# Optimization experiments

Hardware: AMD Instinct MI355X
Metric: run time of the kernel (lower is better)

## Reference

```python
import jax, jax.numpy as jnp
import numpy as np

C, INTER, RED4 = 256, 128, 64  # in_channels, inter_ch=max(C//2,32), C//4

def setup_inputs() -> dict:
    key = jax.random.key(0)
    ks = jax.random.split(key, 12)
    B, H, W = 8, 64, 64
    s = 0.02
    return {
        "x": jax.random.normal(ks[0], (B, C, H, W), dtype=jnp.float32),
        "theta_w": jax.random.normal(ks[1], (INTER, C), dtype=jnp.float32) * s,
        "phi_w": jax.random.normal(ks[2], (INTER, C), dtype=jnp.float32) * s,
        "g_w": jax.random.normal(ks[3], (INTER, C), dtype=jnp.float32) * s,
        "out_w": jax.random.normal(ks[4], (C, INTER), dtype=jnp.float32) * s,
        "bn_gamma": jnp.ones((C,), dtype=jnp.float32),
        "bn_beta": jnp.zeros((C,), dtype=jnp.float32),
        "fc1_w": jax.random.normal(ks[5], (RED4, C), dtype=jnp.float32) * s,
        "fc1_b": jnp.zeros((RED4,), dtype=jnp.float32),
        "fc2_w": jax.random.normal(ks[6], (C, RED4), dtype=jnp.float32) * s,
        "fc2_b": jnp.zeros((C,), dtype=jnp.float32),
    }

def reference(x, theta_w, phi_w, g_w, out_w, bn_gamma, bn_beta, fc1_w, fc1_b, fc2_w, fc2_b):
    B, Cc, H, W = x.shape
    N = H * W
    xf = x.reshape(B, Cc, N)                              # [B,C,N]
    # 1x1 convs == per-pixel matmuls
    theta = jnp.einsum('ic,bcn->bni', theta_w, xf)        # [B,N,I]
    phi = jnp.einsum('ic,bcn->bin', phi_w, xf)            # [B,I,N]
    g = jnp.einsum('ic,bcn->bni', g_w, xf)                # [B,N,I]
    scale = 1.0 / jnp.sqrt(jnp.asarray(theta.shape[-1], theta.dtype))
    attn = jax.nn.softmax(jnp.einsum('bni,bim->bnm', theta, phi) * scale, axis=-1)  # [B,N,N]
    out = jnp.einsum('bnm,bmi->bni', attn, g)             # [B,N,I]
    out = jnp.einsum('ci,bni->bcn', out_w, out).reshape(B, Cc, H, W)
    # BatchNorm2d (training mode: batch stats, biased variance, eps=1e-5)
    mean = out.mean(axis=(0, 2, 3))
    var = out.var(axis=(0, 2, 3))
    out = (out - mean[:, None, None]) * jax.lax.rsqrt(var[:, None, None] + 1e-5)
    out = out * bn_gamma[:, None, None] + bn_beta[:, None, None]
    # SE channel attention on the input x
    pooled = x.mean(axis=(2, 3))                          # [B,C]
    h = jax.nn.relu(pooled @ fc1_w.T + fc1_b)
    ch_w = jax.nn.sigmoid(h @ fc2_w.T + fc2_b)[:, :, None, None]
    return x + out * ch_w
```

## Files before the change

### kernel.cpp

```cpp
#include <hip/hip_runtime.h>

#define B_DIM 8
#define C_DIM 256
#define I_DIM 128
#define N_DIM 4096
#define R_DIM 64

typedef unsigned short u16;
typedef unsigned int u32;
typedef __attribute__((ext_vector_type(8))) __bf16 bf16x8;
typedef __attribute__((ext_vector_type(4))) float f32x4;
typedef __attribute__((ext_vector_type(16))) float f32x16;

union BF8 { u32 u[4]; bf16x8 v; };

__device__ __forceinline__ u16 f2bf(float f) {
    union { float f; u32 u; } v; v.f = f;
    u32 r = v.u + 0x7FFFu + ((v.u >> 16) & 1u);
    return (u16)(r >> 16);
}
__device__ __forceinline__ float bf2f(u16 h) {
    union { u32 u; float f; } v; v.u = (u32)h << 16; return v.f;
}
__device__ __forceinline__ u32 pk2(float a, float b) {
    return (u32)f2bf(a) | ((u32)f2bf(b) << 16);
}
__device__ __forceinline__ u32 pk2t(float a, float b) {
    union { float f; u32 u; } ua, ub; ua.f = a; ub.f = b;
    return __builtin_amdgcn_perm(ub.u, ua.u, 0x07060302u);
}
__device__ __forceinline__ void async16(const u16* g, u16* l) {
    __builtin_amdgcn_global_load_lds((const __attribute__((address_space(1))) void*)g,
                                     (__attribute__((address_space(3))) void*)l, 16, 0, 0);
}

#define TH_SCALE 0.1275204890136f

static constexpr size_t OFF_BNSUM = 0;
static constexpr size_t OFF_BNSQ  = 1024;
static constexpr size_t OFF_POOL  = 2048;
static constexpr size_t OFF_CHW   = 10240;
static constexpr size_t OFF_W3    = 18432;
static constexpr size_t OFF_OWB   = 215040;
static constexpr size_t OFF_AO0   = 280576;
static constexpr size_t OFF_AO1   = OFF_AO0 + 8388608;
static constexpr size_t OFF_THETA = OFF_AO1 + 8388608;
static constexpr size_t OFF_PHIT  = OFF_THETA + 8388608;
static constexpr size_t OFF_GT    = OFF_PHIT + 8388608;
static constexpr size_t OFF_L0    = OFF_GT + 8388608;
static constexpr size_t OFF_L1    = OFF_L0 + 131072;
static constexpr size_t OFF_OUT2  = OFF_L1 + 131072;

__global__ void prep_kernel(const float* __restrict__ tw, const float* __restrict__ pw,
                            const float* __restrict__ gw, const float* __restrict__ ow,
                            u16* __restrict__ w3, u16* __restrict__ owb,
                            float* __restrict__ bnzero, float* __restrict__ pooled) {
    int idx = blockIdx.x * 256 + threadIdx.x;
    if (idx < 512) bnzero[idx] = 0.f;
    if (idx < 2048) pooled[idx] = 0.f;
    if (idx < 3 * 32768) {
        const float* src = idx < 32768 ? tw : (idx < 65536 ? pw : gw);
        w3[idx] = f2bf(src[idx & 32767]);
    }
    if (idx < 32768) owb[idx] = f2bf(ow[idx]);
}

__global__ void se_kernel(const float* __restrict__ pooled,
                          const float* __restrict__ fc1w, const float* __restrict__ fc1b,
                          const float* __restrict__ fc2w, const float* __restrict__ fc2b,
                          float* __restrict__ chw) {
    int b = blockIdx.x, t = threadIdx.x;
    __shared__ float sp[C_DIM], sh[R_DIM];
    sp[t] = pooled[b * C_DIM + t] * (1.f / N_DIM);
    __syncthreads();
    if (t < R_DIM) {
        float a = fc1b[t];
        for (int c = 0; c < C_DIM; ++c) a += sp[c] * fc1w[t * C_DIM + c];
        sh[t] = a > 0.f ? a : 0.f;
    }
    __syncthreads();
    float a = fc2b[t];
    for (int j = 0; j < R_DIM; ++j) a += sh[j] * fc2w[t * R_DIM + j];
    chw[b * C_DIM + t] = 1.f / (1.f + __builtin_amdgcn_exp2f(-a * 1.44269504089f));
}

__global__ __launch_bounds__(256) void qkv_kernel(const float* __restrict__ x,
                                                  const u16* __restrict__ w3,
                                                  u16* __restrict__ theta,
                                                  u16* __restrict__ phiT,
                                                  u16* __restrict__ gT,
                                                  float* __restrict__ pooled) {
    const int bid = blockIdx.x;
    const int b = bid & 7, nt = bid >> 3;
    const int n0 = nt * 64;
    const int t = threadIdx.x, lane = t & 63, w = t >> 6;
    const int cl = lane & 31, h = lane >> 5;

    __shared__ u16 As[64 * 256];
    __shared__ u16 Ep[128 * 72];

    {
        const float* xb = x + ((size_t)b * C_DIM) * N_DIM + n0;
        for (int it = 0; it < 16; ++it) {
            int id = it * 256 + t;
            int c = id >> 4, l16 = id & 15;
            float4 v = *(const float4*)(xb + (size_t)c * N_DIM + l16 * 4);
            int g = c >> 3, co = c & 7;
            float vv[4] = {v.x, v.y, v.z, v.w};
            #pragma unroll
            for (int k = 0; k < 4; ++k) {
                int n = l16 * 4 + k;
                As[n * 256 + ((g ^ (n & 7)) << 3) + co] = f2bf(vv[k]);
            }
            float s = (v.x + v.y) + (v.z + v.w);
            s += __shfl_xor(s, 1); s += __shfl_xor(s, 2);
            s += __shfl_xor(s, 4); s += __shfl_xor(s, 8);
            if ((t & 15) == 0) atomicAdd(&pooled[b * C_DIM + c], s);
        }
    }
    __syncthreads();

    const int mt = w & 1;
    const int ip = w >> 1;
    bf16x8 afr[16];
    #pragma unroll
    for (int ks = 0; ks < 16; ++ks) {
        int r = mt * 32 + cl;
        int g = 2 * ks + h;
        afr[ks] = *(const bf16x8*)&As[r * 256 + ((g ^ (r & 7)) << 3)];
    }

    for (int z = 0; z < 3; ++z) {
        const u16* wz = w3 + z * (I_DIM * C_DIM);
        f32x16 acc[2] = {};
        #pragma unroll
        for (int ks = 0; ks < 16; ++ks) {
            #pragma unroll
            for (int f = 0; f < 2; ++f) {
                int irow = (2 * ip + f) * 32 + cl;
                bf16x8 bfr = *(const bf16x8*)(wz + (size_t)irow * C_DIM + ks * 16 + h * 8);
                acc[f] = __builtin_amdgcn_mfma_f32_32x32x16_bf16(afr[ks], bfr, acc[f], 0, 0, 0);
            }
        }
        if (z < 2) {
            float sc = (z == 0) ? TH_SCALE : 1.0f;
            #pragma unroll
            for (int f = 0; f < 2; ++f) {
                int i = (2 * ip + f) * 32 + cl;
                #pragma unroll
                for (int r2 = 0; r2 < 4; ++r2)
                    #pragma unroll
                    for (int e = 0; e < 4; ++e) {
                        int n = mt * 32 + 8 * r2 + 4 * h + e;
                        Ep[n * 136 + i] = f2bf(acc[f][4 * r2 + e] * sc);
                    }
            }
            __syncthreads();
            u16* dst = (z == 0) ? theta : phiT;
            #pragma unroll
            for (int it = 0; it < 4; ++it) {
                int id = it * 256 + t;
                int n = id >> 4, l16 = id & 15;
                f32x4 vv = *(const f32x4*)&Ep[n * 136 + l16 * 8];
                *(f32x4*)(dst + ((size_t)(b * N_DIM) + n0 + n) * I_DIM + l16 * 8) = vv;
            }
            __syncthreads();
        } else {
            #pragma unroll
            for (int f = 0; f < 2; ++f) {
                int i = (2 * ip + f) * 32 + cl;
                #pragma unroll
                for (int r2 = 0; r2 < 4; ++r2) {
                    u32 lo = pk2(acc[f][4 * r2 + 0], acc[f][4 * r2 + 1]);
                    u32 hi = pk2(acc[f][4 * r2 + 2], acc[f][4 * r2 + 3]);
                    int nb = mt * 32 + 8 * r2 + 4 * h;
                    *(u32*)&Ep[i * 72 + nb] = lo;
                    *(u32*)&Ep[i * 72 + nb + 2] = hi;
                }
            }
            __syncthreads();
            #pragma unroll
            for (int it = 0; it < 4; ++it) {
                int id = it * 256 + t;
                int i = id >> 3, l8 = id & 7;
                f32x4 vv = *(const f32x4*)&Ep[i * 72 + l8 * 8];
                *(f32x4*)(gT + ((size_t)(b * I_DIM) + i) * N_DIM + n0 + l8 * 8) = vv;
            }
        }
    }
}

__global__ __launch_bounds__(256) void attn_kernel(const u16* __restrict__ theta,
                                                   const u16* __restrict__ phiT,
                                                   const u16* __restrict__ gT,
                                                   u16* __restrict__ ao0, u16* __restrict__ ao1,
                                                   float* __restrict__ l0, float* __restrict__ l1) {
    const int bid = blockIdx.x;
    const int b = bid & 7, mh = (bid >> 3) & 1, qt = bid >> 4;
    const int t = threadIdx.x, lane = t & 63, w = t >> 6;
    const int cl = lane & 31, h = lane >> 5;
    const int qw = qt * 128 + w * 32;

    __shared__ u16 SM[32768];
    __shared__ float lex[4][32];

    bf16x8 qf[8];
    {
        const u16* qp = theta + ((size_t)(b * N_DIM) + qw + cl) * I_DIM + h * 8;
        #pragma unroll
        for (int ks = 0; ks < 8; ++ks) qf[ks] = *(const bf16x8*)(qp + ks * 16);
    }

    const u16* kbase = phiT + (size_t)b * N_DIM * I_DIM + (size_t)(mh * 2048) * I_DIM;
    const u16* vbase = gT + (size_t)b * I_DIM * N_DIM + mh * 2048;
    const u16* kptr[4]; const u16* vptr[4];
    #pragma unroll
    for (int it = 0; it < 4; ++it) {
        int gi = (w * 4 + it) * 64 + lane;
        int kr = gi >> 4, kg = gi & 15;
        kptr[it] = kbase + (size_t)kr * I_DIM + ((kg ^ (kr & 7)) << 3);
        int vr = gi >> 3, vg = gi & 7;
        vptr[it] = vbase + (size_t)vr * N_DIM + ((vg ^ (vr & 7)) << 3);
    }

    auto issue = [&](int p) {
        u16* Kd = SM + p * 16384;
        u16* Vd = SM + p * 16384 + 8192;
        #pragma unroll
        for (int it = 0; it < 4; ++it) { async16(kptr[it], Kd + (w * 4 + it) * 512); kptr[it] += 64 * I_DIM; }
        #pragma unroll
        for (int it = 0; it < 4; ++it) { async16(vptr[it], Vd + (w * 4 + it) * 512); vptr[it] += 64; }
    };

    float lsum = 0.f;
    f32x16 O[4] = {};

    issue(0);

    for (int mc = 0; mc < 32; ++mc) {
        const int p = mc & 1;
        __asm__ volatile("s_barrier" ::: "memory");
        if (mc < 31) {
            issue(1 - p);
            __asm__ volatile("s_waitcnt vmcnt(8)" ::: "memory");
        } else {
            __asm__ volatile("s_waitcnt vmcnt(0)" ::: "memory");
        }
        __asm__ volatile("s_barrier" ::: "memory");

        const u16* Ks = SM + p * 16384;
        const u16* Vs = SM + p * 16384 + 8192;

        u32 pk[8][2];
        #pragma unroll
        for (int mt2 = 0; mt2 < 2; ++mt2) {
            f32x16 S = {};
            #pragma unroll
            for (int ks = 0; ks < 8; ++ks) {
                int r = mt2 * 32 + cl;
                bf16x8 kf = *(const bf16x8*)&Ks[r * 128 + (((2 * ks + h) ^ (r & 7)) << 3)];
                S = __builtin_amdgcn_mfma_f32_32x32x16_bf16(kf, qf[ks], S, 0, 0, 0);
            }
            #pragma unroll
            for (int r2 = 0; r2 < 4; ++r2) {
                float p0 = __builtin_amdgcn_exp2f(S[4 * r2 + 0]);
                float p1 = __builtin_amdgcn_exp2f(S[4 * r2 + 1]);
                float p2 = __builtin_amdgcn_exp2f(S[4 * r2 + 2]);
                float p3 = __builtin_amdgcn_exp2f(S[4 * r2 + 3]);
                lsum += (p0 + p1) + (p2 + p3);
                pk[mt2 * 4 + r2][0] = pk2t(p0, p1);
                pk[mt2 * 4 + r2][1] = pk2t(p2, p3);
            }
        }

        #pragma unroll
        for (int ks = 0; ks < 4; ++ks) {
            u32 a0 = pk[2 * ks][0], a1 = pk[2 * ks][1];
            u32 b0 = pk[2 * ks + 1][0], b1 = pk[2 * ks + 1][1];
            bool hb = (h != 0);
            u32 own0 = hb ? b0 : a0, own1 = hb ? b1 : a1;
            u32 xf0 = hb ? a0 : b0, xf1 = hb ? a1 : b1;
            u32 rc0 = (u32)__shfl_xor((int)xf0, 32);
            u32 rc1 = (u32)__shfl_xor((int)xf1, 32);
            BF8 A;
            A.u[0] = hb ? rc0 : own0;
            A.u[1] = hb ? rc1 : own1;
            A.u[2] = hb ? own0 : rc0;
            A.u[3] = hb ? own1 : rc1;
            #pragma unroll
            for (int f = 0; f < 4; ++f) {
                int ir = f * 32 + cl;
                bf16x8 vf = *(const bf16x8*)&Vs[ir * 64 + (((2 * ks + h) ^ (ir & 7)) << 3)];
                O[f] = __builtin_amdgcn_mfma_f32_32x32x16_bf16(A.v, vf, O[f], 0, 0, 0);
            }
        }
    }

    lsum += __shfl_xor(lsum, 32);
    if (h == 0) lex[w][cl] = lsum;
    __asm__ volatile("s_waitcnt lgkmcnt(0)" ::: "memory");

    float linv[16];
    {
        float* lw = lex[w];
        #pragma unroll
        for (int r2 = 0; r2 < 4; ++r2) {
            f32x4 lv = *(const f32x4*)&lw[8 * r2 + 4 * h];
            #pragma unroll
            for (int e = 0; e < 4; ++e) linv[4 * r2 + e] = 1.f / lv[e];
        }
    }

    u16* aop = (mh == 0) ? ao0 : ao1;
    float* lp = (mh == 0) ? l0 : l1;
    if (h == 0) lp[(size_t)b * N_DIM + qw + cl] = lsum;

    u16* ep = SM + w * 4096;
    #pragma unroll
    for (int f = 0; f < 4; ++f)
        #pragma unroll
        for (int r2 = 0; r2 < 4; ++r2)
            #pragma unroll
            for (int e = 0; e < 4; ++e) {
                int q = 8 * r2 + 4 * h + e;
                ep[q * 128 + f * 32 + cl] = f2bf(O[f][4 * r2 + e] * linv[4 * r2 + e]);
            }
    __asm__ volatile("s_waitcnt lgkmcnt(0)" ::: "memory");
    #pragma unroll
    for (int it = 0; it < 8; ++it) {
        int id = it * 64 + lane;
        int q = id >> 4, l16 = id & 15;
        f32x4 vv = *(const f32x4*)&ep[q * 128 + l16 * 8];
        *(f32x4*)(aop + ((size_t)(b * N_DIM) + qw + q) * I_DIM + l16 * 8) = vv;
    }
}

__global__ __launch_bounds__(256) void oproj_kernel(const u16* __restrict__ ao0,
                                                    const u16* __restrict__ ao1,
                                                    const float* __restrict__ l0,
                                                    const float* __restrict__ l1,
                                                    const u16* __restrict__ owb,
                                                    u16* __restrict__ out2,
                                                    float* __restrict__ bnsum,
                                                    float* __restrict__ bnsumsq) {
    const int bid = blockIdx.x;
    const int b = bid & 7, nt = bid >> 3;
    const int n0 = nt * 64;
    const int t = threadIdx.x, lane = t & 63, w = t >> 6;
    const int cl = lane & 31, h = lane >> 5;

    __shared__ u16 Ep[256 * 72];
    __shared__ float lsum[C_DIM], lsq[C_DIM];
    lsum[t] = 0.f; lsq[t] = 0.f;
    __syncthreads();

    const int mt = w & 1;
    const int nn = n0 + mt * 32 + cl;
    float w0, w1;
    {
        float la = l0[(size_t)b * N_DIM + nn], lb = l1[(size_t)b * N_DIM + nn];
        float inv = 1.f / (la + lb);
        w0 = la * inv; w1 = lb * inv;
    }
    bf16x8 afr[8];
    {
        const u16* p0 = ao0 + ((size_t)(b * N_DIM) + nn) * I_DIM + h * 8;
        const u16* p1 = ao1 + ((size_t)(b * N_DIM) + nn) * I_DIM + h * 8;
        #pragma unroll
        for (int ks = 0; ks < 8; ++ks) {
            bf16x8 x0 = *(const bf16x8*)(p0 + ks * 16);
            bf16x8 x1 = *(const bf16x8*)(p1 + ks * 16);
            const u16* u0 = (const u16*)&x0;
            const u16* u1 = (const u16*)&x1;
            float c0 = w0 * bf2f(u0[0]) + w1 * bf2f(u1[0]);
            float c1 = w0 * bf2f(u0[1]) + w1 * bf2f(u1[1]);
            float c2 = w0 * bf2f(u0[2]) + w1 * bf2f(u1[2]);
            float c3 = w0 * bf2f(u0[3]) + w1 * bf2f(u1[3]);
            float c4 = w0 * bf2f(u0[4]) + w1 * bf2f(u1[4]);
            float c5 = w0 * bf2f(u0[5]) + w1 * bf2f(u1[5]);
            float c6 = w0 * bf2f(u0[6]) + w1 * bf2f(u1[6]);
            float c7 = w0 * bf2f(u0[7]) + w1 * bf2f(u1[7]);
            BF8 r;
            r.u[0] = pk2(c0, c1); r.u[1] = pk2(c2, c3);
            r.u[2] = pk2(c4, c5); r.u[3] = pk2(c6, c7);
            afr[ks] = r.v;
        }
    }

    f32x16 D[4] = {};
    #pragma unroll
    for (int ks = 0; ks < 8; ++ks) {
        #pragma unroll
        for (int j = 0; j < 4; ++j) {
            int cr = ((w >> 1) * 4 + j) * 32 + cl;
            bf16x8 bfr = *(const bf16x8*)(owb + (size_t)cr * I_DIM + ks * 16 + h * 8);
            D[j] = __builtin_amdgcn_mfma_f32_32x32x16_bf16(afr[ks], bfr, D[j], 0, 0, 0);
        }
    }

    #pragma unroll
    for (int j = 0; j < 4; ++j) {
        int c = ((w >> 1) * 4 + j) * 32 + cl;
        float s1 = 0.f, s2 = 0.f;
        #pragma unroll
        for (int r2 = 0; r2 < 4; ++r2) {
            float v0 = D[j][4 * r2 + 0], v1 = D[j][4 * r2 + 1];
            float v2 = D[j][4 * r2 + 2], v3 = D[j][4 * r2 + 3];
            s1 += (v0 + v1) + (v2 + v3);
            s2 += (v0 * v0 + v1 * v1) + (v2 * v2 + v3 * v3);
            int nb = mt * 32 + 8 * r2 + 4 * h;
            *(u32*)&Ep[c * 72 + nb] = pk2(v0, v1);
            *(u32*)&Ep[c * 72 + nb + 2] = pk2(v2, v3);
        }
        atomicAdd(&lsum[c], s1);
        atomicAdd(&lsq[c], s2);
    }
    __syncthreads();
    #pragma unroll
    for (int it = 0; it < 8; ++it) {
        int id = it * 256 + t;
        int c = id >> 3, l8 = id & 7;
        f32x4 vv = *(const f32x4*)&Ep[c * 72 + l8 * 8];
        *(f32x4*)(out2 + ((size_t)(b * C_DIM) + c) * N_DIM + n0 + l8 * 8) = vv;
    }
    atomicAdd(&bnsum[t], lsum[t]);
    atomicAdd(&bnsumsq[t], lsq[t]);
}

__global__ void final_kernel(const float* __restrict__ x, const u16* __restrict__ out2,
                             const float* __restrict__ bnsum, const float* __restrict__ bnsumsq,
                             const float* __restrict__ gamma, const float* __restrict__ beta,
                             const float* __restrict__ chw, float* __restrict__ out) {
    int idx = blockIdx.x * 256 + threadIdx.x;
    int e = idx * 4;
    int b = e >> 20;
    int c = (e >> 12) & 255;
    float mean = bnsum[c] * (1.f / 32768.f);
    float var = bnsumsq[c] * (1.f / 32768.f) - mean * mean;
    float sc = gamma[c] * rsqrtf(var + 1e-5f);
    float sh = beta[c] - mean * sc;
    float cw = chw[b * C_DIM + c];
    ushort4 o16 = ((const ushort4*)out2)[idx];
    float4 xv = ((const float4*)x)[idx];
    float4 res;
    res.x = xv.x + (bf2f(o16.x) * sc + sh) * cw;
    res.y = xv.y + (bf2f(o16.y) * sc + sh) * cw;
    res.z = xv.z + (bf2f(o16.z) * sc + sh) * cw;
    res.w = xv.w + (bf2f(o16.w) * sc + sh) * cw;
    ((float4*)out)[idx] = res;
}

extern "C" void kernel_launch(void* const* d_in, const int* in_sizes, int n_in,
                              void* d_out, int out_size, void* d_ws, size_t ws_size,
                              hipStream_t stream) {
    const float* x   = (const float*)d_in[0];
    const float* tw  = (const float*)d_in[1];
    const float* pw  = (const float*)d_in[2];
    const float* gw  = (const float*)d_in[3];
    const float* ow  = (const float*)d_in[4];
    const float* gam = (const float*)d_in[5];
    const float* bet = (const float*)d_in[6];
    const float* f1w = (const float*)d_in[7];
    const float* f1b = (const float*)d_in[8];
    const float* f2w = (const float*)d_in[9];
    const float* f2b = (const float*)d_in[10];
    float* out = (float*)d_out;

    char* ws = (char*)d_ws;
    float* bnsum   = (float*)(ws + OFF_BNSUM);
    float* bnsumsq = (float*)(ws + OFF_BNSQ);
    float* pooled  = (float*)(ws + OFF_POOL);
    float* chw     = (float*)(ws + OFF_CHW);
    u16*   w3      = (u16*)(ws + OFF_W3);
    u16*   owb     = (u16*)(ws + OFF_OWB);
    u16*   ao0     = (u16*)(ws + OFF_AO0);
    u16*   ao1     = (u16*)(ws + OFF_AO1);
    u16*   theta   = (u16*)(ws + OFF_THETA);
    u16*   phiT    = (u16*)(ws + OFF_PHIT);
    u16*   gT      = (u16*)(ws + OFF_GT);
    float* l0      = (float*)(ws + OFF_L0);
    float* l1      = (float*)(ws + OFF_L1);
    u16*   out2    = (u16*)(ws + OFF_OUT2);

    prep_kernel<<<384, 256, 0, stream>>>(tw, pw, gw, ow, w3, owb, bnsum, pooled);
    qkv_kernel<<<512, 256, 0, stream>>>(x, w3, theta, phiT, gT, pooled);
    se_kernel<<<B_DIM, 256, 0, stream>>>(pooled, f1w, f1b, f2w, f2b, chw);
    attn_kernel<<<512, 256, 0, stream>>>(theta, phiT, gT, ao0, ao1, l0, l1);
    oproj_kernel<<<512, 256, 0, stream>>>(ao0, ao1, l0, l1, owb, out2, bnsum, bnsumsq);
    final_kernel<<<8192, 256, 0, stream>>>(x, out2, bnsum, bnsumsq, gam, bet, chw, out);
}
```

Before: 270.4 us.

## Fuse QKV projections into one pass and defer softmax normalization to oproj

The QKV kernel now writes x to shared memory as packed bf16 pairs through lane shuffles and byte permutes, with an adjusted swizzle. It then computes theta, phi and g in one fused MFMA loop over six accumulators and stages all outputs through one shared buffer before storing, instead of three sequential passes with syncs. The attention kernel no longer divides its output by the partial row sum, removing a shared-memory exchange. The projection kernel merges the two halves as (a0+a1)/(l0+l1). This raises register pressure and stores unnormalized bf16 partial outputs, which may lose some precision.

```diff
diff --git a/kernel.cpp b/kernel.cpp
--- a/kernel.cpp
+++ b/kernel.cpp
@@ -96,8 +96,10 @@
     const int t = threadIdx.x, lane = t & 63, w = t >> 6;
     const int cl = lane & 31, h = lane >> 5;
 
-    __shared__ u16 As[64 * 256];
-    __shared__ u16 Ep[128 * 72];
+    __shared__ u16 SMQ[26624];
+    u16* As  = SMQ;
+    u16* Ep  = SMQ;
+    u16* EpG = SMQ + 17408;
 
     {
         const float* xb = x + ((size_t)b * C_DIM) * N_DIM + n0;
@@ -105,17 +107,26 @@
             int id = it * 256 + t;
             int c = id >> 4, l16 = id & 15;
             float4 v = *(const float4*)(xb + (size_t)c * N_DIM + l16 * 4);
-            int g = c >> 3, co = c & 7;
-            float vv[4] = {v.x, v.y, v.z, v.w};
-            #pragma unroll
-            for (int k = 0; k < 4; ++k) {
-                int n = l16 * 4 + k;
-                As[n * 256 + ((g ^ (n & 7)) << 3) + co] = f2bf(vv[k]);
-            }
             float s = (v.x + v.y) + (v.z + v.w);
             s += __shfl_xor(s, 1); s += __shfl_xor(s, 2);
             s += __shfl_xor(s, 4); s += __shfl_xor(s, 8);
             if ((t & 15) == 0) atomicAdd(&pooled[b * C_DIM + c], s);
+            u32 lo = pk2t(v.x, v.y), hi = pk2t(v.z, v.w);
+            u32 plo = (u32)__shfl_xor((int)lo, 16);
+            u32 phi2 = (u32)__shfl_xor((int)hi, 16);
+            u32 w0, w1; int nrow, cp;
+            if ((c & 1) == 0) {
+                w0 = __builtin_amdgcn_perm(plo, lo, 0x05040100u);
+                w1 = __builtin_amdgcn_perm(plo, lo, 0x07060302u);
+                nrow = 4 * l16; cp = c;
+            } else {
+                w0 = __builtin_amdgcn_perm(hi, phi2, 0x05040100u);
+                w1 = __builtin_amdgcn_perm(hi, phi2, 0x07060302u);
+                nrow = 4 * l16 + 2; cp = c - 1;
+            }
+            int base = (((cp >> 3) ^ (l16 & 7)) << 3) + (cp & 7);
+            *(u32*)&As[nrow * 256 + base] = w0;
+            *(u32*)&As[(nrow + 1) * 256 + base] = w1;
         }
     }
     __syncthreads();
@@ -127,66 +138,61 @@
     for (int ks = 0; ks < 16; ++ks) {
         int r = mt * 32 + cl;
         int g = 2 * ks + h;
-        afr[ks] = *(const bf16x8*)&As[r * 256 + ((g ^ (r & 7)) << 3)];
-    }
-
-    for (int z = 0; z < 3; ++z) {
-        const u16* wz = w3 + z * (I_DIM * C_DIM);
-        f32x16 acc[2] = {};
-        #pragma unroll
-        for (int ks = 0; ks < 16; ++ks) {
+        afr[ks] = *(const bf16x8*)&As[r * 256 + ((g ^ ((r >> 2) & 7)) << 3)];
+    }
+    __syncthreads();
+
+    f32x16 acc[6] = {};
+    const u16* wz0 = w3;
+    const u16* wz1 = w3 + 32768;
+    const u16* wz2 = w3 + 65536;
+    #pragma unroll
+    for (int ks = 0; ks < 16; ++ks) {
+        bf16x8 a = afr[ks];
+        #pragma unroll
+        for (int f = 0; f < 2; ++f) {
+            size_t off = (size_t)((2 * ip + f) * 32 + cl) * C_DIM + ks * 16 + h * 8;
+            acc[f]     = __builtin_amdgcn_mfma_f32_32x32x16_bf16(a, *(const bf16x8*)(wz0 + off), acc[f], 0, 0, 0);
+            acc[2 + f] = __builtin_amdgcn_mfma_f32_32x32x16_bf16(a, *(const bf16x8*)(wz1 + off), acc[2 + f], 0, 0, 0);
+            acc[4 + f] = __builtin_amdgcn_mfma_f32_32x32x16_bf16(a, *(const bf16x8*)(wz2 + off), acc[4 + f], 0, 0, 0);
+        }
+    }
+
+    #pragma unroll
+    for (int f = 0; f < 2; ++f) {
+        int i = (2 * ip + f) * 32 + cl;
+        #pragma unroll
+        for (int r2 = 0; r2 < 4; ++r2) {
             #pragma unroll
-            for (int f = 0; f < 2; ++f) {
-                int irow = (2 * ip + f) * 32 + cl;
-                bf16x8 bfr = *(const bf16x8*)(wz + (size_t)irow * C_DIM + ks * 16 + h * 8);
-                acc[f] = __builtin_amdgcn_mfma_f32_32x32x16_bf16(afr[ks], bfr, acc[f], 0, 0, 0);
-            }
-        }
-        if (z < 2) {
-            float sc = (z == 0) ? TH_SCALE : 1.0f;
-            #pragma unroll
-            for (int f = 0; f < 2; ++f) {
-                int i = (2 * ip + f) * 32 + cl;
-                #pragma unroll
-                for (int r2 = 0; r2 < 4; ++r2)
-                    #pragma unroll
-                    for (int e = 0; e < 4; ++e) {
-                        int n = mt * 32 + 8 * r2 + 4 * h + e;
-                        Ep[n * 136 + i] = f2bf(acc[f][4 * r2 + e] * sc);
-                    }
-            }
-            __syncthreads();
-            u16* dst = (z == 0) ? theta : phiT;
-            #pragma unroll
-            for (int it = 0; it < 4; ++it) {
-                int id = it * 256 + t;
-                int n = id >> 4, l16 = id & 15;
-                f32x4 vv = *(const f32x4*)&Ep[n * 136 + l16 * 8];
-                *(f32x4*)(dst + ((size_t)(b * N_DIM) + n0 + n) * I_DIM + l16 * 8) = vv;
-            }
-            __syncthreads();
-        } else {
-            #pragma unroll
-            for (int f = 0; f < 2; ++f) {
-                int i = (2 * ip + f) * 32 + cl;
-                #pragma unroll
-                for (int r2 = 0; r2 < 4; ++r2) {
-                    u32 lo = pk2(acc[f][4 * r2 + 0], acc[f][4 * r2 + 1]);
-                    u32 hi = pk2(acc[f][4 * r2 + 2], acc[f][4 * r2 + 3]);
-                    int nb = mt * 32 + 8 * r2 + 4 * h;
-                    *(u32*)&Ep[i * 72 + nb] = lo;
-                    *(u32*)&Ep[i * 72 + nb + 2] = hi;
-                }
-            }
-            __syncthreads();
-            #pragma unroll
-            for (int it = 0; it < 4; ++it) {
-                int id = it * 256 + t;
-                int i = id >> 3, l8 = id & 7;
-                f32x4 vv = *(const f32x4*)&Ep[i * 72 + l8 * 8];
-                *(f32x4*)(gT + ((size_t)(b * I_DIM) + i) * N_DIM + n0 + l8 * 8) = vv;
-            }
-        }
+            for (int e = 0; e < 4; ++e) {
+                int n = mt * 32 + 8 * r2 + 4 * h + e;
+                Ep[n * 136 + i] = f2bf(acc[f][4 * r2 + e] * TH_SCALE);
+                Ep[(64 + n) * 136 + i] = f2bf(acc[2 + f][4 * r2 + e]);
+            }
+            u32 lo = pk2(acc[4 + f][4 * r2 + 0], acc[4 + f][4 * r2 + 1]);
+            u32 hi = pk2(acc[4 + f][4 * r2 + 2], acc[4 + f][4 * r2 + 3]);
+            int nb = mt * 32 + 8 * r2 + 4 * h;
+            *(u32*)&EpG[i * 72 + nb] = lo;
+            *(u32*)&EpG[i * 72 + nb + 2] = hi;
+        }
+    }
+    __syncthreads();
+
+    #pragma unroll
+    for (int it = 0; it < 8; ++it) {
+        int id = it * 256 + t;
+        int row = id >> 4, l16 = id & 15;
+        f32x4 vv = *(const f32x4*)&Ep[row * 136 + l16 * 8];
+        u16* dst = (row < 64) ? theta : phiT;
+        int n = row & 63;
+        *(f32x4*)(dst + ((size_t)(b * N_DIM) + n0 + n) * I_DIM + l16 * 8) = vv;
+    }
+    #pragma unroll
+    for (int it = 0; it < 4; ++it) {
+        int id = it * 256 + t;
+        int i = id >> 3, l8 = id & 7;
+        f32x4 vv = *(const f32x4*)&EpG[i * 72 + l8 * 8];
+        *(f32x4*)(gT + ((size_t)(b * I_DIM) + i) * N_DIM + n0 + l8 * 8) = vv;
     }
 }
 
@@ -202,7 +208,6 @@
     const int qw = qt * 128 + w * 32;
 
     __shared__ u16 SM[32768];
-    __shared__ float lex[4][32];
 
     bf16x8 qf[8];
     {
@@ -297,20 +302,6 @@
     }
 
     lsum += __shfl_xor(lsum, 32);
-    if (h == 0) lex[w][cl] = lsum;
-    __asm__ volatile("s_waitcnt lgkmcnt(0)" ::: "memory");
-
-    float linv[16];
-    {
-        float* lw = lex[w];
-        #pragma unroll
-        for (int r2 = 0; r2 < 4; ++r2) {
-            f32x4 lv = *(const f32x4*)&lw[8 * r2 + 4 * h];
-            #pragma unroll
-            for (int e = 0; e < 4; ++e) linv[4 * r2 + e] = 1.f / lv[e];
-        }
-    }
-
     u16* aop = (mh == 0) ? ao0 : ao1;
     float* lp = (mh == 0) ? l0 : l1;
     if (h == 0) lp[(size_t)b * N_DIM + qw + cl] = lsum;
@@ -323,7 +314,7 @@
             #pragma unroll
             for (int e = 0; e < 4; ++e) {
                 int q = 8 * r2 + 4 * h + e;
-                ep[q * 128 + f * 32 + cl] = f2bf(O[f][4 * r2 + e] * linv[4 * r2 + e]);
+                ep[q * 128 + f * 32 + cl] = f2bf(O[f][4 * r2 + e]);
             }
     __asm__ volatile("s_waitcnt lgkmcnt(0)" ::: "memory");
     #pragma unroll
@@ -356,11 +347,10 @@
 
     const int mt = w & 1;
     const int nn = n0 + mt * 32 + cl;
-    float w0, w1;
+    float inv;
     {
         float la = l0[(size_t)b * N_DIM + nn], lb = l1[(size_t)b * N_DIM + nn];
-        float inv = 1.f / (la + lb);
-        w0 = la * inv; w1 = lb * inv;
+        inv = 1.f / (la + lb);
     }
     bf16x8 afr[8];
     {
@@ -372,14 +362,14 @@
             bf16x8 x1 = *(const bf16x8*)(p1 + ks * 16);
             const u16* u0 = (const u16*)&x0;
             const u16* u1 = (const u16*)&x1;
-            float c0 = w0 * bf2f(u0[0]) + w1 * bf2f(u1[0]);
-            float c1 = w0 * bf2f(u0[1]) + w1 * bf2f(u1[1]);
-            float c2 = w0 * bf2f(u0[2]) + w1 * bf2f(u1[2]);
-            float c3 = w0 * bf2f(u0[3]) + w1 * bf2f(u1[3]);
-            float c4 = w0 * bf2f(u0[4]) + w1 * bf2f(u1[4]);
-            float c5 = w0 * bf2f(u0[5]) + w1 * bf2f(u1[5]);
-            float c6 = w0 * bf2f(u0[6]) + w1 * bf2f(u1[6]);
-            float c7 = w0 * bf2f(u0[7]) + w1 * bf2f(u1[7]);
+            float c0 = (bf2f(u0[0]) + bf2f(u1[0])) * inv;
+            float c1 = (bf2f(u0[1]) + bf2f(u1[1])) * inv;
+            float c2 = (bf2f(u0[2]) + bf2f(u1[2])) * inv;
+            float c3 = (bf2f(u0[3]) + bf2f(u1[3])) * inv;
+            float c4 = (bf2f(u0[4]) + bf2f(u1[4])) * inv;
+            float c5 = (bf2f(u0[5]) + bf2f(u1[5])) * inv;
+            float c6 = (bf2f(u0[6]) + bf2f(u1[6])) * inv;
+            float c7 = (bf2f(u0[7]) + bf2f(u1[7])) * inv;
             BF8 r;
             r.u[0] = pk2(c0, c1); r.u[1] = pk2(c2, c3);
             r.u[2] = pk2(c4, c5); r.u[3] = pk2(c6, c7);
```

Result: no change. 275.2 us (+1.8%).
